# Performance work log

Hardware: AMD Instinct MI355X
Metric: run time of the kernel (lower is better)

Reference implementation:

```python
import jax, jax.numpy as jnp
import numpy as np
import math

HIDDEN = 1024
N_HEADS = 16
HEAD_DIM = HIDDEN // N_HEADS
N_BLOCKS = 16
BATCH = 2
SEQ = 4096


def setup_inputs() -> dict:
    key = jax.random.key(0)
    ks = jax.random.split(key, 8)
    attention_input = jax.random.normal(ks[0], (BATCH, SEQ, HIDDEN), dtype=jnp.float32)
    attention_mask = jnp.ones((BATCH, SEQ), dtype=jnp.float32)
    # permutation over the num_blocks*num_heads flattened (block, head) axis
    permutation = jax.random.permutation(ks[1], N_BLOCKS * N_HEADS)
    init = 0.02
    q_w = jax.random.normal(ks[2], (HIDDEN, N_HEADS, HEAD_DIM), dtype=jnp.float32) * init
    q_b = jax.random.normal(ks[3], (N_HEADS, HEAD_DIM), dtype=jnp.float32) * init
    k_w = jax.random.normal(ks[4], (HIDDEN, N_HEADS, HEAD_DIM), dtype=jnp.float32) * init
    k_b = jax.random.normal(ks[5], (N_HEADS, HEAD_DIM), dtype=jnp.float32) * init
    v_w = jax.random.normal(ks[6], (HIDDEN, N_HEADS, HEAD_DIM), dtype=jnp.float32) * init
    v_b = jax.random.normal(ks[7], (N_HEADS, HEAD_DIM), dtype=jnp.float32) * init
    return {"attention_input": attention_input, "attention_mask": attention_mask,
            "permutation": permutation, "q_w": q_w, "q_b": q_b,
            "k_w": k_w, "k_b": k_b, "v_w": v_w, "v_b": v_b}


def reference(attention_input, attention_mask, permutation, q_w, q_b, k_w, k_b, v_w, v_b):
    B = attention_mask.shape[0]
    S = attention_mask.shape[1]
    nb = N_BLOCKS
    nh, d = q_b.shape
    blk = S // nb
    # QKV projections: [B,S,H] x [H,N,D] -> [B,S,N,D]
    q = jnp.einsum('bsh,hnd->bsnd', attention_input, q_w) + q_b
    k = jnp.einsum('bsh,hnd->bsnd', attention_input, k_w) + k_b
    v = jnp.einsum('bsh,hnd->bsnd', attention_input, v_w) + v_b

    def blockify(x):  # [B,S,N,D] -> [B, nb, nh, blk, d]
        return x.reshape(B, nb, blk, nh, d).transpose(0, 1, 3, 2, 4)

    q = blockify(q)
    # flatten (block, head) axis and gather per permutation
    k = blockify(k).reshape(B, nb * nh, blk, d)[:, permutation].reshape(B, nb, nh, blk, d)
    v = blockify(v).reshape(B, nb * nh, blk, d)[:, permutation].reshape(B, nb, nh, blk, d)

    scale = 1.0 / math.sqrt(float(d))
    logits = jnp.einsum('bgnqd,bgnkd->bgnqk', q, k) * scale  # block-local scores
    attn = jax.nn.softmax(logits, axis=-1)  # dropout prob 0 / eval mode
    ctx = jnp.einsum('bgnqk,bgnkd->bgnqd', attn, v)
    # [B,nb,nh,blk,d] -> [B,nb,blk,nh,d] -> [B,S,nh,d]
    return ctx.transpose(0, 1, 3, 2, 4).reshape(B, S, nh, d)
```

## Files before the change

kernel.cpp:

```cpp
#include <hip/hip_runtime.h>
#include <hip/hip_bf16.h>
#include <stdint.h>

typedef __attribute__((ext_vector_type(4))) float f32x4;
typedef __attribute__((ext_vector_type(8))) short s16x8;

__device__ inline short f2bf(float f) {
  union { float f; uint32_t u; } v; v.f = f;
  uint32_t r = v.u + 0x7fffu + ((v.u >> 16) & 1u);
  return (short)(r >> 16);
}

__device__ inline void gload_lds16(const void* g, void* l) {
  __builtin_amdgcn_global_load_lds((const __attribute__((address_space(1))) void*)g,
                                   (__attribute__((address_space(3))) void*)l,
                                   16, 0, 0);
}

#define MFMA16 __builtin_amdgcn_mfma_f32_16x16x32_bf16

__global__ __launch_bounds__(256) void k_prep(const float* __restrict__ x,
                                              short* __restrict__ xb,
                                              const float* __restrict__ qw,
                                              const float* __restrict__ kw,
                                              const float* __restrict__ vw,
                                              short* __restrict__ wt) {
  __shared__ float tile[64][65];
  int bx = blockIdx.x;
  if (bx < 4096) {
    int i = (bx * 256 + threadIdx.x) * 8;
    const float4* p = (const float4*)(x + i);
    float4 a = p[0], b = p[1];
    s16x8 o;
    o[0] = f2bf(a.x); o[1] = f2bf(a.y); o[2] = f2bf(a.z); o[3] = f2bf(a.w);
    o[4] = f2bf(b.x); o[5] = f2bf(b.y); o[6] = f2bf(b.z); o[7] = f2bf(b.w);
    *(s16x8*)(xb + i) = o;
    return;
  }
  bx -= 4096;
  int a  = bx >> 8;
  int t2 = bx & 255;
  int k0 = (t2 >> 4) << 6;
  int n0 = (t2 & 15) << 6;
  const float* w = (a == 0) ? qw : (a == 1) ? kw : vw;
  int c = threadIdx.x & 63, rr = threadIdx.x >> 6;
#pragma unroll
  for (int i = 0; i < 16; ++i) {
    int r = i * 4 + rr;
    tile[r][c] = w[(k0 + r) * 1024 + n0 + c];
  }
  __syncthreads();
  short* o = wt + a * 1048576;
#pragma unroll
  for (int i = 0; i < 16; ++i) {
    int r = i * 4 + rr;
    o[(n0 + r) * 1024 + k0 + c] = f2bf(tile[c][r]);
  }
}

__global__ __launch_bounds__(256, 2) void k_gemm(const short* __restrict__ xb,
                                                 const short* __restrict__ wt,
                                                 const float* __restrict__ qbias,
                                                 const float* __restrict__ kbias,
                                                 const float* __restrict__ vbias,
                                                 short* __restrict__ Qo,
                                                 short* __restrict__ Ko,
                                                 short* __restrict__ Vo) {
  __shared__ short lds[36864];
  const int tid = threadIdx.x, lane = tid & 63, wv = tid >> 6;
  const int wm = wv >> 1, wn = wv & 1;
  const int mt = blockIdx.x, by = blockIdx.y;
  const int a = by >> 3;
  const short* asrc = xb + (size_t)(mt * 256) * 1024;
  const short* bsrc = wt + (size_t)a * 1048576 + (size_t)((by & 7) * 128) * 1024;

  int srcA[4], dstA[4], srcB[2], dstB[2];
#pragma unroll
  for (int i = 0; i < 4; ++i) {
    int L = i * 256 + tid, s = L & 31;
    int row = (L >> 5) * 8 + (s >> 2);
    int c = (s & 3) ^ ((s >> 3) & 3);
    srcA[i] = row * 1024 + c * 8;
    dstA[i] = L * 16;
  }
#pragma unroll
  for (int i = 0; i < 2; ++i) {
    int L = i * 256 + tid, s = L & 31;
    int row = (L >> 5) * 8 + (s >> 2);
    int c = (s & 3) ^ ((s >> 3) & 3);
    srcB[i] = row * 1024 + c * 8;
    dstB[i] = 16384 + L * 16;
  }

  int aoff[8], boff[4];
#pragma unroll
  for (int m = 0; m < 8; ++m) {
    int row = wm * 128 + m * 16 + (lane & 15);
    aoff[m] = ((row >> 3) * 32 + (row & 7) * 4 + ((lane >> 4) ^ ((row >> 1) & 3))) * 16;
  }
#pragma unroll
  for (int n = 0; n < 4; ++n) {
    int row = wn * 64 + n * 16 + (lane & 15);
    boff[n] = 16384 + ((row >> 3) * 32 + (row & 7) * 4 + ((lane >> 4) ^ ((row >> 1) & 3))) * 16;
  }

  f32x4 acc[8][4] = {};

  auto STAGE = [&](int t, int bb) {
    const short* at = asrc + t * 32;
    const short* bt = bsrc + t * 32;
    char* l = (char*)lds + bb;
#pragma unroll
    for (int i = 0; i < 4; ++i) gload_lds16(at + srcA[i], l + dstA[i]);
#pragma unroll
    for (int i = 0; i < 2; ++i) gload_lds16(bt + srcB[i], l + dstB[i]);
  };

  STAGE(0, 0);
  STAGE(1, 24576);
  int bcur = 0, bpre = 49152;

  for (int t = 0; t < 31; ++t) {
    asm volatile("s_waitcnt vmcnt(6)" ::: "memory");
    __builtin_amdgcn_s_barrier();
    asm volatile("" ::: "memory");
    if (t < 30) STAGE(t + 2, bpre);
    const char* bufc = (const char*)lds + bcur;
    s16x8 af[8], bf[4];
#pragma unroll
    for (int m = 0; m < 8; ++m) af[m] = *(const s16x8*)(bufc + aoff[m]);
#pragma unroll
    for (int n = 0; n < 4; ++n) bf[n] = *(const s16x8*)(bufc + boff[n]);
    __builtin_amdgcn_s_setprio(1);
#pragma unroll
    for (int m = 0; m < 8; ++m)
#pragma unroll
      for (int n = 0; n < 4; ++n)
        acc[m][n] = MFMA16(af[m], bf[n], acc[m][n], 0, 0, 0);
    __builtin_amdgcn_s_setprio(0);
    bcur += 24576; if (bcur == 73728) bcur = 0;
    bpre += 24576; if (bpre == 73728) bpre = 0;
  }
  asm volatile("s_waitcnt vmcnt(0)" ::: "memory");
  __builtin_amdgcn_s_barrier();
  asm volatile("" ::: "memory");
  {
    const char* bufc = (const char*)lds + bcur;
    s16x8 af[8], bf[4];
#pragma unroll
    for (int m = 0; m < 8; ++m) af[m] = *(const s16x8*)(bufc + aoff[m]);
#pragma unroll
    for (int n = 0; n < 4; ++n) bf[n] = *(const s16x8*)(bufc + boff[n]);
    __builtin_amdgcn_s_setprio(1);
#pragma unroll
    for (int m = 0; m < 8; ++m)
#pragma unroll
      for (int n = 0; n < 4; ++n)
        acc[m][n] = MFMA16(af[m], bf[n], acc[m][n], 0, 0, 0);
    __builtin_amdgcn_s_setprio(0);
  }

  const float* bias = (a == 0) ? qbias : (a == 1) ? kbias : vbias;
  short* outp = (a == 0) ? Qo : (a == 1) ? Ko : Vo;
  int nbase = (by & 7) * 128 + wn * 64;
  int mbase = mt * 256 + wm * 128;
#pragma unroll
  for (int n = 0; n < 4; ++n) {
    int nloc = nbase + n * 16 + (lane & 15);
    float bv = bias[nloc];
#pragma unroll
    for (int m = 0; m < 8; ++m)
#pragma unroll
      for (int r = 0; r < 4; ++r) {
        int mm = mbase + m * 16 + ((lane >> 4) << 2) + r;
        outp[(size_t)mm * 1024 + nloc] = f2bf(acc[m][n][r] + bv);
      }
  }
}

__global__ __launch_bounds__(256, 2) void k_attn(const short* __restrict__ Qb,
                                                 const short* __restrict__ Kb,
                                                 const short* __restrict__ Vb,
                                                 const int* __restrict__ perm,
                                                 float* __restrict__ out) {
  __shared__ short Ks[256 * 64];
  __shared__ short Vs[64 * 256];
  __shared__ short Ps[4 * 1024];

  int tid = threadIdx.x;
  int lane = tid & 63, wv = tid >> 6;
  int bx = blockIdx.x;
  int wg = (bx & 7) * 128 + (bx >> 3);
  int b = wg >> 9, g = (wg >> 5) & 15, n = (wg >> 1) & 15, h = wg & 1;
  int p = perm[g * 16 + n];
  int pg = p >> 4, ph = p & 15;

  const short* qsrc = Qb + (size_t)(b * 4096 + g * 256 + h * 128) * 1024 + n * 64;
  const short* ksrc = Kb + (size_t)(b * 4096 + pg * 256) * 1024 + ph * 64;
  const short* vsrc = Vb + (size_t)(b * 4096 + pg * 256) * 1024 + ph * 64;

  int qr0 = wv * 32;

#pragma unroll
  for (int i = 0; i < 8; ++i) {
    int c = i * 256 + tid;
    int row = c >> 3;
    int sc = ((c & 7) << 4) ^ ((row & 7) << 4);
    gload_lds16(ksrc + row * 1024 + (sc >> 1), (char*)Ks + c * 16);
  }
  __builtin_amdgcn_sched_barrier(0);
  s16x8 vreg[8];
#pragma unroll
  for (int i = 0; i < 8; ++i) {
    int c = i * 256 + tid;
    int t = c >> 3;
    int d0 = (c & 7) << 3;
    vreg[i] = *(const s16x8*)(vsrc + t * 1024 + d0);
  }
  s16x8 qreg[2][2];
#pragma unroll
  for (int rf = 0; rf < 2; ++rf)
#pragma unroll
    for (int ks = 0; ks < 2; ++ks) {
      int row = qr0 + rf * 16 + (lane & 15);
      qreg[rf][ks] = *(const s16x8*)(qsrc + row * 1024 + ks * 32 + ((lane >> 4) << 3));
    }
  __builtin_amdgcn_sched_barrier(0);
  asm volatile("s_waitcnt vmcnt(12)" ::: "memory");
  __builtin_amdgcn_s_barrier();
  __builtin_amdgcn_sched_barrier(0);

  f32x4 accS[2][16] = {};
#pragma unroll
  for (int ks = 0; ks < 2; ++ks) {
    int cb = (ks << 6) + ((lane >> 4) << 4);
#pragma unroll
    for (int cf = 0; cf < 16; ++cf) {
      int row = cf * 16 + (lane & 15);
      s16x8 bk = *(const s16x8*)((const char*)Ks + row * 128 + (cb ^ ((row & 7) << 4)));
      accS[0][cf] = MFMA16(qreg[0][ks], bk, accS[0][cf], 0, 0, 0);
      accS[1][cf] = MFMA16(qreg[1][ks], bk, accS[1][cf], 0, 0, 0);
    }
  }

#pragma unroll
  for (int i = 0; i < 8; ++i) {
    int c = i * 256 + tid;
    int t = c >> 3;
    int d0 = (c & 7) << 3;
#pragma unroll
    for (int j = 0; j < 8; ++j) {
      int d = d0 + j;
      int sl = (d & 7) ^ ((d >> 3) & 7);
      int by = d * 512 + ((t * 2) ^ (sl << 4));
      *(short*)((char*)Vs + by) = vreg[i][j];
    }
  }
  __syncthreads();

  const float sc_log2e = 0.125f * 1.44269504088896f;
  float mx[2][4], inv[2][4];
#pragma unroll
  for (int rf = 0; rf < 2; ++rf)
#pragma unroll
    for (int r = 0; r < 4; ++r) {
      float m_ = accS[rf][0][r];
#pragma unroll
      for (int cf = 1; cf < 16; ++cf) m_ = fmaxf(m_, accS[rf][cf][r]);
#pragma unroll
      for (int msk = 1; msk < 16; msk <<= 1) m_ = fmaxf(m_, __shfl_xor(m_, msk));
      mx[rf][r] = m_;
    }
#pragma unroll
  for (int rf = 0; rf < 2; ++rf)
#pragma unroll
    for (int r = 0; r < 4; ++r) {
      float s_ = 0.f;
#pragma unroll
      for (int cf = 0; cf < 16; ++cf) {
        float e = exp2f((accS[rf][cf][r] - mx[rf][r]) * sc_log2e);
        accS[rf][cf][r] = e;
        s_ += e;
      }
#pragma unroll
      for (int msk = 1; msk < 16; msk <<= 1) s_ += __shfl_xor(s_, msk);
      inv[rf][r] = 1.0f / s_;
    }

  f32x4 accO[2][4] = {};
  short* pchunk = Ps + wv * 1024;
#pragma unroll
  for (int ks = 0; ks < 8; ++ks) {
#pragma unroll
    for (int rf = 0; rf < 2; ++rf)
#pragma unroll
      for (int half = 0; half < 2; ++half) {
        int cf = ks * 2 + half;
        int kvl = half * 16 + (lane & 15);
        int qp = (lane >> 4) << 2;
        int base = rf * 512 + ((kvl >> 3) << 7) + (kvl & 7);
#pragma unroll
        for (int r = 0; r < 4; ++r)
          pchunk[base + (qp + r) * 8] = f2bf(accS[rf][cf][r]);
      }
    int cbv = (ks << 6) + ((lane >> 4) << 4);
#pragma unroll
    for (int rf = 0; rf < 2; ++rf) {
      s16x8 ap = *(const s16x8*)(pchunk + rf * 512 + lane * 8);
#pragma unroll
      for (int dc = 0; dc < 4; ++dc) {
        int vrow = dc * 16 + (lane & 15);
        int sl = (vrow & 7) ^ ((vrow >> 3) & 7);
        s16x8 bv = *(const s16x8*)((const char*)Vs + vrow * 512 + (cbv ^ (sl << 4)));
        accO[rf][dc] = MFMA16(ap, bv, accO[rf][dc], 0, 0, 0);
      }
    }
  }

#pragma unroll
  for (int rf = 0; rf < 2; ++rf)
#pragma unroll
    for (int dc = 0; dc < 4; ++dc)
#pragma unroll
      for (int r = 0; r < 4; ++r) {
        int q = h * 128 + qr0 + rf * 16 + ((lane >> 4) << 2) + r;
        int d = dc * 16 + (lane & 15);
        out[(size_t)((b * 4096 + g * 256 + q) * 16 + n) * 64 + d] = accO[rf][dc][r] * inv[rf][r];
      }
}

extern "C" void kernel_launch(void* const* d_in, const int* in_sizes, int n_in,
                              void* d_out, int out_size, void* d_ws, size_t ws_size,
                              hipStream_t stream) {
  const float* x    = (const float*)d_in[0];
  const int*   perm = (const int*)d_in[2];
  const float* qw   = (const float*)d_in[3];
  const float* qb   = (const float*)d_in[4];
  const float* kw   = (const float*)d_in[5];
  const float* kb   = (const float*)d_in[6];
  const float* vw   = (const float*)d_in[7];
  const float* vb   = (const float*)d_in[8];
  float* out = (float*)d_out;

  char* ws = (char*)d_ws;
  short* Xb = (short*)(ws);
  short* Wt = (short*)(ws + 16777216UL);
  short* Qb = (short*)(ws + 23068672UL);
  short* Kb = (short*)(ws + 39845888UL);
  short* Vb = (short*)(ws + 56623104UL);

  k_prep<<<4864, 256, 0, stream>>>(x, Xb, qw, kw, vw, Wt);
  k_gemm<<<dim3(32, 24), 256, 0, stream>>>(Xb, Wt, qb, kb, vb, Qb, Kb, Vb);
  k_attn<<<1024, 256, 0, stream>>>(Qb, Kb, Vb, perm, out);
}
```

Before: 99.56 us.

## Split attention KV into two halves with online softmax to raise occupancy

```diff
diff --git a/kernel.cpp b/kernel.cpp
--- a/kernel.cpp
+++ b/kernel.cpp
@@ -178,13 +178,13 @@
   }
 }
 
-__global__ __launch_bounds__(256, 2) void k_attn(const short* __restrict__ Qb,
+__global__ __launch_bounds__(256, 3) void k_attn(const short* __restrict__ Qb,
                                                  const short* __restrict__ Kb,
                                                  const short* __restrict__ Vb,
                                                  const int* __restrict__ perm,
                                                  float* __restrict__ out) {
-  __shared__ short Ks[256 * 64];
-  __shared__ short Vs[64 * 256];
+  __shared__ short Ks[128 * 64];
+  __shared__ short Vt[64 * 128];
   __shared__ short Ps[4 * 1024];
 
   int tid = threadIdx.x;
@@ -201,22 +201,30 @@
 
   int qr0 = wv * 32;
 
-#pragma unroll
-  for (int i = 0; i < 8; ++i) {
-    int c = i * 256 + tid;
-    int row = c >> 3;
-    int sc = ((c & 7) << 4) ^ ((row & 7) << 4);
-    gload_lds16(ksrc + row * 1024 + (sc >> 1), (char*)Ks + c * 16);
-  }
+  auto STAGE_K = [&](int hf) {
+#pragma unroll
+    for (int i = 0; i < 4; ++i) {
+      int c = i * 256 + tid;
+      int row = c >> 3;
+      int sc = ((c & 7) << 4) ^ ((row & 7) << 4);
+      gload_lds16(ksrc + (size_t)(hf * 128 + row) * 1024 + (sc >> 1), (char*)Ks + c * 16);
+    }
+  };
+
+  s16x8 vreg[4];
+  auto LOAD_V = [&](int hf) {
+#pragma unroll
+    for (int i = 0; i < 4; ++i) {
+      int c = i * 256 + tid;
+      int t = c >> 3;
+      int d0 = (c & 7) << 3;
+      vreg[i] = *(const s16x8*)(vsrc + (size_t)(hf * 128 + t) * 1024 + d0);
+    }
+  };
+
+  STAGE_K(0);
   __builtin_amdgcn_sched_barrier(0);
-  s16x8 vreg[8];
-#pragma unroll
-  for (int i = 0; i < 8; ++i) {
-    int c = i * 256 + tid;
-    int t = c >> 3;
-    int d0 = (c & 7) << 3;
-    vreg[i] = *(const s16x8*)(vsrc + t * 1024 + d0);
-  }
+  LOAD_V(0);
   s16x8 qreg[2][2];
 #pragma unroll
   for (int rf = 0; rf < 2; ++rf)
@@ -226,97 +234,125 @@
       qreg[rf][ks] = *(const s16x8*)(qsrc + row * 1024 + ks * 32 + ((lane >> 4) << 3));
     }
   __builtin_amdgcn_sched_barrier(0);
-  asm volatile("s_waitcnt vmcnt(12)" ::: "memory");
-  __builtin_amdgcn_s_barrier();
-  __builtin_amdgcn_sched_barrier(0);
-
-  f32x4 accS[2][16] = {};
-#pragma unroll
-  for (int ks = 0; ks < 2; ++ks) {
-    int cb = (ks << 6) + ((lane >> 4) << 4);
-#pragma unroll
-    for (int cf = 0; cf < 16; ++cf) {
-      int row = cf * 16 + (lane & 15);
-      s16x8 bk = *(const s16x8*)((const char*)Ks + row * 128 + (cb ^ ((row & 7) << 4)));
-      accS[0][cf] = MFMA16(qreg[0][ks], bk, accS[0][cf], 0, 0, 0);
-      accS[1][cf] = MFMA16(qreg[1][ks], bk, accS[1][cf], 0, 0, 0);
-    }
-  }
-
-#pragma unroll
-  for (int i = 0; i < 8; ++i) {
-    int c = i * 256 + tid;
-    int t = c >> 3;
-    int d0 = (c & 7) << 3;
-#pragma unroll
-    for (int j = 0; j < 8; ++j) {
-      int d = d0 + j;
-      int sl = (d & 7) ^ ((d >> 3) & 7);
-      int by = d * 512 + ((t * 2) ^ (sl << 4));
-      *(short*)((char*)Vs + by) = vreg[i][j];
-    }
-  }
-  __syncthreads();
 
   const float sc_log2e = 0.125f * 1.44269504088896f;
-  float mx[2][4], inv[2][4];
+  float m_run[2][4], l_run[2][4];
+  f32x4 accO[2][4] = {};
 #pragma unroll
   for (int rf = 0; rf < 2; ++rf)
 #pragma unroll
-    for (int r = 0; r < 4; ++r) {
-      float m_ = accS[rf][0][r];
-#pragma unroll
-      for (int cf = 1; cf < 16; ++cf) m_ = fmaxf(m_, accS[rf][cf][r]);
-#pragma unroll
-      for (int msk = 1; msk < 16; msk <<= 1) m_ = fmaxf(m_, __shfl_xor(m_, msk));
-      mx[rf][r] = m_;
-    }
-#pragma unroll
-  for (int rf = 0; rf < 2; ++rf)
-#pragma unroll
-    for (int r = 0; r < 4; ++r) {
-      float s_ = 0.f;
-#pragma unroll
-      for (int cf = 0; cf < 16; ++cf) {
-        float e = exp2f((accS[rf][cf][r] - mx[rf][r]) * sc_log2e);
-        accS[rf][cf][r] = e;
-        s_ += e;
-      }
-#pragma unroll
-      for (int msk = 1; msk < 16; msk <<= 1) s_ += __shfl_xor(s_, msk);
-      inv[rf][r] = 1.0f / s_;
-    }
-
-  f32x4 accO[2][4] = {};
-  short* pchunk = Ps + wv * 1024;
-#pragma unroll
-  for (int ks = 0; ks < 8; ++ks) {
+    for (int r = 0; r < 4; ++r) { m_run[rf][r] = -3.0e38f; l_run[rf][r] = 0.f; }
+
+#pragma unroll
+  for (int hf = 0; hf < 2; ++hf) {
+    if (hf == 0) { asm volatile("s_waitcnt vmcnt(8)" ::: "memory"); }
+    else         { asm volatile("s_waitcnt vmcnt(4)" ::: "memory"); }
+    __builtin_amdgcn_s_barrier();
+    __builtin_amdgcn_sched_barrier(0);
+
+    f32x4 accS[2][8];
 #pragma unroll
     for (int rf = 0; rf < 2; ++rf)
 #pragma unroll
-      for (int half = 0; half < 2; ++half) {
-        int cf = ks * 2 + half;
-        int kvl = half * 16 + (lane & 15);
-        int qp = (lane >> 4) << 2;
-        int base = rf * 512 + ((kvl >> 3) << 7) + (kvl & 7);
-#pragma unroll
-        for (int r = 0; r < 4; ++r)
-          pchunk[base + (qp + r) * 8] = f2bf(accS[rf][cf][r]);
-      }
-    int cbv = (ks << 6) + ((lane >> 4) << 4);
-#pragma unroll
-    for (int rf = 0; rf < 2; ++rf) {
-      s16x8 ap = *(const s16x8*)(pchunk + rf * 512 + lane * 8);
+      for (int cf = 0; cf < 8; ++cf) accS[rf][cf] = (f32x4){0.f, 0.f, 0.f, 0.f};
+#pragma unroll
+    for (int ks = 0; ks < 2; ++ks) {
+      int cb = (ks << 6) + ((lane >> 4) << 4);
+#pragma unroll
+      for (int cf = 0; cf < 8; ++cf) {
+        int row = cf * 16 + (lane & 15);
+        s16x8 bk = *(const s16x8*)((const char*)Ks + row * 128 + (cb ^ ((row & 7) << 4)));
+        accS[0][cf] = MFMA16(qreg[0][ks], bk, accS[0][cf], 0, 0, 0);
+        accS[1][cf] = MFMA16(qreg[1][ks], bk, accS[1][cf], 0, 0, 0);
+      }
+    }
+
+#pragma unroll
+    for (int i = 0; i < 4; ++i) {
+      int c = i * 256 + tid;
+      int t = c >> 3;
+      int d0 = (c & 7) << 3;
+#pragma unroll
+      for (int j = 0; j < 8; ++j) {
+        int d = d0 + j;
+        int p4 = (((d & 7) ^ ((d >> 3) & 7)) << 1) | ((d >> 3) & 1);
+        *(short*)((char*)Vt + d * 256 + ((t * 2) ^ (p4 << 4))) = vreg[i][j];
+      }
+    }
+
+#pragma unroll
+    for (int rf = 0; rf < 2; ++rf)
+#pragma unroll
+      for (int r = 0; r < 4; ++r) {
+        float pm = accS[rf][0][r];
+#pragma unroll
+        for (int cf = 1; cf < 8; ++cf) pm = fmaxf(pm, accS[rf][cf][r]);
+#pragma unroll
+        for (int msk = 1; msk < 16; msk <<= 1) pm = fmaxf(pm, __shfl_xor(pm, msk));
+        float m_new = fmaxf(m_run[rf][r], pm);
+        float sc = exp2f((m_run[rf][r] - m_new) * sc_log2e);
+        float s_ = 0.f;
+#pragma unroll
+        for (int cf = 0; cf < 8; ++cf) {
+          float e = exp2f((accS[rf][cf][r] - m_new) * sc_log2e);
+          accS[rf][cf][r] = e;
+          s_ += e;
+        }
+#pragma unroll
+        for (int msk = 1; msk < 16; msk <<= 1) s_ += __shfl_xor(s_, msk);
+        l_run[rf][r] = l_run[rf][r] * sc + s_;
+        m_run[rf][r] = m_new;
+#pragma unroll
+        for (int dc = 0; dc < 4; ++dc) accO[rf][dc][r] *= sc;
+      }
+
+    __builtin_amdgcn_s_barrier();
+    __builtin_amdgcn_sched_barrier(0);
+    if (hf == 0) {
+      STAGE_K(1);
+      __builtin_amdgcn_sched_barrier(0);
+      LOAD_V(1);
+      __builtin_amdgcn_sched_barrier(0);
+    }
+
+    short* pchunk = Ps + wv * 1024;
+#pragma unroll
+    for (int ks = 0; ks < 4; ++ks) {
+#pragma unroll
+      for (int rf = 0; rf < 2; ++rf)
+#pragma unroll
+        for (int hk = 0; hk < 2; ++hk) {
+          int cf = ks * 2 + hk;
+          int kvl = hk * 16 + (lane & 15);
+          int qp = (lane >> 4) << 2;
+          int base = rf * 512 + ((kvl >> 3) << 7) + (kvl & 7);
+#pragma unroll
+          for (int r = 0; r < 4; ++r)
+            pchunk[base + (qp + r) * 8] = f2bf(accS[rf][cf][r]);
+        }
+      int cbv = (ks << 6) + ((lane >> 4) << 4);
+      s16x8 bv[4];
 #pragma unroll
       for (int dc = 0; dc < 4; ++dc) {
         int vrow = dc * 16 + (lane & 15);
-        int sl = (vrow & 7) ^ ((vrow >> 3) & 7);
-        s16x8 bv = *(const s16x8*)((const char*)Vs + vrow * 512 + (cbv ^ (sl << 4)));
-        accO[rf][dc] = MFMA16(ap, bv, accO[rf][dc], 0, 0, 0);
-      }
-    }
-  }
-
+        int p4 = (((vrow & 7) ^ ((vrow >> 3) & 7)) << 1) | ((vrow >> 3) & 1);
+        bv[dc] = *(const s16x8*)((const char*)Vt + vrow * 256 + (cbv ^ (p4 << 4)));
+      }
+#pragma unroll
+      for (int rf = 0; rf < 2; ++rf) {
+        s16x8 ap = *(const s16x8*)(pchunk + rf * 512 + lane * 8);
+#pragma unroll
+        for (int dc = 0; dc < 4; ++dc)
+          accO[rf][dc] = MFMA16(ap, bv[dc], accO[rf][dc], 0, 0, 0);
+      }
+    }
+  }
+
+  float inv[2][4];
+#pragma unroll
+  for (int rf = 0; rf < 2; ++rf)
+#pragma unroll
+    for (int r = 0; r < 4; ++r) inv[rf][r] = 1.0f / l_run[rf][r];
 #pragma unroll
   for (int rf = 0; rf < 2; ++rf)
 #pragma unroll
```

Result: slower. 134.1 us (+34.6%).
